# Optimization experiments

Measured on AMD Instinct MI355X. Metric: run time of the kernel, lower is better.

## Reference

```python
import jax, jax.numpy as jnp
import numpy as np

N_EMBD = 1024
N_HEAD = 16
HEAD_SIZE = N_EMBD // N_HEAD


def setup_inputs() -> dict:
    key = jax.random.key(0)
    k_x, k_w, k_b = jax.random.split(key, 3)
    B, T, C = 2, 2048, N_EMBD
    x = jax.random.normal(k_x, (B, T, C), dtype=jnp.float32)
    # Linear(n_embd, 3*n_embd): weight [C, 3C] (applied as x @ W), bias [3C]
    w_qkv = jax.random.normal(k_w, (C, 3 * C), dtype=jnp.float32) * (1.0 / np.sqrt(C))
    b_qkv = jax.random.normal(k_b, (3 * C,), dtype=jnp.float32) * 0.02
    return {"x": x, "w_qkv": w_qkv, "b_qkv": b_qkv}


def reference(x, w_qkv, b_qkv):
    B, T, C = x.shape
    H, D = N_HEAD, HEAD_SIZE
    qkv = x @ w_qkv + b_qkv                      # [B, T, 3C]
    q, k, v = jnp.split(qkv, 3, axis=-1)         # each [B, T, C]
    # [B, T, C] -> [B, H, T, D]
    q = q.reshape(B, T, H, D).transpose(0, 2, 1, 3)
    k = k.reshape(B, T, H, D).transpose(0, 2, 1, 3)
    v = v.reshape(B, T, H, D).transpose(0, 2, 1, 3)
    scores = jnp.einsum('bhqd,bhkd->bhqk', q, k) / jnp.sqrt(jnp.float32(D))
    causal = jnp.tril(jnp.ones((T, T), dtype=bool))  # allow j <= i
    scores = jnp.where(causal[None, None, :, :], scores, -jnp.inf)
    weights = jax.nn.softmax(scores, axis=-1)    # [B, H, T, T]
    out = jnp.einsum('bhqk,bhkd->bhqd', weights, v)
    out = out.transpose(0, 2, 1, 3).reshape(B, T, C)
    return out
```

## Files before the change

kernel.cpp:

```cpp
#include <hip/hip_runtime.h>
#include <hip/hip_bf16.h>


#define CDIM  1024
#define C3    3072
#define HS    64
#define TLEN  2048
#define KVT   64
#define SCL   0.1803368801111204f

typedef __attribute__((ext_vector_type(8))) short bf16x8;
typedef __attribute__((ext_vector_type(4))) float f32x4;
typedef __attribute__((ext_vector_type(4))) unsigned short u16x4;

__device__ __forceinline__ unsigned short f2b(float f) {
    unsigned u = __float_as_uint(f);
    unsigned r = (u + 0x7FFFu + ((u >> 16) & 1u)) >> 16;
    return (unsigned short)r;
}
__device__ __forceinline__ float b2f(unsigned short u) {
    return __uint_as_float(((unsigned)u) << 16);
}
__device__ __forceinline__ float fexp2(float x) {
    return __builtin_amdgcn_exp2f(x);
}
__device__ __forceinline__ unsigned pkbf(float a, float b) {
    float2 f; f.x = a; f.y = b;
    __hip_bfloat162 h = __float22bfloat162_rn(f);
    union { __hip_bfloat162 h2; unsigned u; } c;
    c.h2 = h;
    return c.u;
}
__device__ __forceinline__ void gl_lds16(const unsigned short* g, unsigned short* l) {
    __builtin_amdgcn_global_load_lds((const __attribute__((address_space(1))) void*)g,
                                     (__attribute__((address_space(3))) void*)l, 16, 0, 0);
}
__device__ __forceinline__ int detect_bf(const void* bias, int lane) {
    unsigned w = ((const unsigned*)bias)[lane];
    unsigned e = (w >> 7) & 0xFF;
    unsigned long long m = __ballot(e >= 100 && e <= 135);
    return __popcll(m) >= 48;
}

__device__ __forceinline__ void plswap(unsigned x, unsigned& y0, unsigned& y1) {
    unsigned aa = x, bb = x;
    asm("v_permlane32_swap_b32 %0, %1" : "+v"(aa), "+v"(bb));
    asm("v_permlane16_swap_b32 %0, %1" : "+v"(aa), "+v"(bb));
    y0 = aa; y1 = bb;
}
__device__ __forceinline__ bf16x8 xfrag(unsigned x00, unsigned x01,
                                        unsigned x10, unsigned x11, int qsel) {
    unsigned y000, y100, y001, y101, y010, y110, y011, y111;
    plswap(x00, y000, y100);
    plswap(x01, y001, y101);
    plswap(x10, y010, y110);
    plswap(x11, y011, y111);
    union { unsigned u[4]; bf16x8 v; } r;
    r.u[0] = qsel ? y010 : y000;
    r.u[1] = qsel ? y011 : y001;
    r.u[2] = qsel ? y110 : y100;
    r.u[3] = qsel ? y111 : y101;
    return r.v;
}

__global__ __launch_bounds__(256) void k_prep(const void* __restrict__ w,
                                              const void* __restrict__ x,
                                              const void* __restrict__ bias,
                                              unsigned short* __restrict__ wt,
                                              unsigned short* __restrict__ xb) {
    __shared__ unsigned short tile[64 * 66];
    int t = threadIdx.x;
    int isbf = detect_bf(bias, t & 63);
    int bid = blockIdx.x;

    {
        int n0 = (bid % 48) * 64;
        int k0 = (bid / 48) * 64;
        for (int i = 0; i < 16; ++i) {
            int idx = t + i * 256;
            int r = idx >> 6, c = idx & 63;
            unsigned short v;
            if (isbf) v = ((const unsigned short*)w)[(k0 + r) * C3 + n0 + c];
            else      v = f2b(((const float*)w)[(k0 + r) * C3 + n0 + c]);
            tile[r * 66 + c] = v;
        }
        __syncthreads();
        for (int i = 0; i < 16; ++i) {
            int idx = t + i * 256;
            int r = idx >> 6, c = idx & 63;
            wt[(n0 + r) * CDIM + k0 + c] = tile[c * 66 + r];
        }
    }
    if (!isbf) {
        const float* s = (const float*)x;
        unsigned* d = (unsigned*)xb;
        for (int sb = bid; sb < 2048; sb += 768) {
            int base = sb * 1024;
            for (int j = t; j < 1024; j += 256) {
                int idx = base + j;
                float a = s[2 * idx], b = s[2 * idx + 1];
                d[idx] = (unsigned)f2b(a) | ((unsigned)f2b(b) << 16);
            }
        }
    }
}

__global__ __launch_bounds__(256, 3) void k_gemm_qkv(const void* __restrict__ xraw,
                                                     const unsigned short* __restrict__ xb,
                                                     const void* __restrict__ biasraw,
                                                     const unsigned short* __restrict__ Bt,
                                                     unsigned short* __restrict__ qk,
                                                     unsigned short* __restrict__ k2,
                                                     unsigned short* __restrict__ v2) {
    __shared__ __align__(16) unsigned short As[2 * 128 * 32];
    __shared__ __align__(16) unsigned short Bs[2 * 128 * 32];
    int tid  = threadIdx.x;
    int lane = tid & 63, wv = tid >> 6;
    int quad = lane >> 4, l16 = lane & 15;
    int isbf = detect_bf(biasraw, lane);
    const unsigned short* A = isbf ? (const unsigned short*)xraw : xb;

    int lin = blockIdx.x + 24 * blockIdx.y;
    int swz = (lin & 7) * 96 + (lin >> 3);
    int m0 = (swz / 24) * 128, n0 = (swz % 24) * 128;
    int wm = (wv >> 1) * 64, wn = (wv & 1) * 64;

    f32x4 acc[4][4] = {};

    int r0 = tid >> 2;
    int g0 = (((tid & 3) ^ (r0 & 3)) * 8);
    const unsigned short* a0 = A  + (m0 + r0) * CDIM + g0;
    const unsigned short* b0 = Bt + (n0 + r0) * CDIM + g0;
    unsigned short* dA = As + tid * 8;
    unsigned short* dB = Bs + tid * 8;

    int sw4 = l16 & 3;
    int aro = (wm + l16) * 32 + ((quad ^ sw4) * 8);
    int bro = (wn + l16) * 32 + ((quad ^ sw4) * 8);

    gl_lds16(a0,                 dA);
    gl_lds16(a0 + 64 * CDIM,     dA + 2048);
    gl_lds16(b0,                 dB);
    gl_lds16(b0 + 64 * CDIM,     dB + 2048);
    gl_lds16(a0 + 32,            dA + 4096);
    gl_lds16(a0 + 64 * CDIM + 32, dA + 4096 + 2048);
    gl_lds16(b0 + 32,            dB + 4096);
    gl_lds16(b0 + 64 * CDIM + 32, dB + 4096 + 2048);
    asm volatile("s_waitcnt vmcnt(4)" ::: "memory");
    __builtin_amdgcn_s_barrier();

    #pragma unroll 2
    for (int kt = 0; kt < 32; ++kt) {
        int cur = kt & 1;
        const unsigned short* Ac = As + cur * 4096;
        const unsigned short* Bc = Bs + cur * 4096;

        bf16x8 af[4], bfv[4];
        #pragma unroll
        for (int mt = 0; mt < 4; ++mt)
            af[mt] = *(const bf16x8*)&Ac[aro + mt * 512];
        #pragma unroll
        for (int nt = 0; nt < 4; ++nt)
            bfv[nt] = *(const bf16x8*)&Bc[bro + nt * 512];

        __builtin_amdgcn_s_setprio(1);
        #pragma unroll
        for (int mt = 0; mt < 4; ++mt)
            #pragma unroll
            for (int nt = 0; nt < 4; ++nt)
                acc[mt][nt] = __builtin_amdgcn_mfma_f32_16x16x32_bf16(af[mt], bfv[nt], acc[mt][nt], 0, 0, 0);
        __builtin_amdgcn_s_setprio(0);

        __builtin_amdgcn_s_barrier();
        if (kt < 30) {
            int koff = (kt + 2) * 32;
            unsigned short* tA = As + cur * 4096;
            unsigned short* tB = Bs + cur * 4096;
            gl_lds16(a0 + koff,            tA + tid * 8);
            gl_lds16(a0 + 64 * CDIM + koff, tA + tid * 8 + 2048);
            gl_lds16(b0 + koff,            tB + tid * 8);
            gl_lds16(b0 + 64 * CDIM + koff, tB + tid * 8 + 2048);
            asm volatile("s_waitcnt vmcnt(4)" ::: "memory");
        } else {
            asm volatile("s_waitcnt vmcnt(0)" ::: "memory");
        }
        __builtin_amdgcn_s_barrier();
    }

    if (n0 < 1024) {
        for (int mt = 0; mt < 4; ++mt) {
            int row = m0 + wm + mt * 16 + quad * 4;
            for (int nt = 0; nt < 4; ++nt) {
                int col = n0 + wn + nt * 16 + l16;
                float bv = isbf ? b2f(((const unsigned short*)biasraw)[col])
                                : ((const float*)biasraw)[col];
                for (int i = 0; i < 4; ++i)
                    qk[(row + i) * 2048 + col] = f2b(acc[mt][nt][i] + bv);
            }
        }
    } else if (n0 < 2048) {
        for (int mt = 0; mt < 4; ++mt) {
            int row = m0 + wm + mt * 16 + quad * 4;
            int tq = row & 2047, b = row >> 11;
            for (int nt = 0; nt < 4; ++nt) {
                int col = n0 + wn + nt * 16 + l16;
                float bv = isbf ? b2f(((const unsigned short*)biasraw)[col])
                                : ((const float*)biasraw)[col];
                int c = col - 1024;
                int hh = c >> 6, d = c & 63;
                int base = ((b * 16 + hh) * 32 + (tq >> 6)) * 4096
                         + ((tq >> 5) & 1) * 2048 + ((tq >> 4) & 1) * 1024
                         + (d >> 5) * 512 + ((d >> 3) & 3) * 128
                         + (tq & 15) * 8 + (d & 7);
                for (int i = 0; i < 4; ++i)
                    k2[base + i * 8] = f2b(acc[mt][nt][i] + bv);
            }
        }
    } else {
        for (int mt = 0; mt < 4; ++mt) {
            int row = m0 + wm + mt * 16 + quad * 4;
            int tq = row & 2047, b = row >> 11;
            for (int nt = 0; nt < 4; ++nt) {
                int col = n0 + wn + nt * 16 + l16;
                float bv = isbf ? b2f(((const unsigned short*)biasraw)[col])
                                : ((const float*)biasraw)[col];
                int c = col - 2048;
                int hh = c >> 6, d = c & 63;
                int base = ((b * 16 + hh) * 32 + (tq >> 6)) * 4096
                         + ((tq >> 5) & 1) * 2048 + (d >> 4) * 512
                         + ((tq >> 3) & 3) * 128 + (d & 15) * 8 + (tq & 7);
                u16x4 pk;
                for (int i = 0; i < 4; ++i) pk[i] = f2b(acc[mt][nt][i] + bv);
                *(u16x4*)&v2[base] = pk;
            }
        }
    }
}

__global__ __launch_bounds__(256, 4) void k_attn(const unsigned short* __restrict__ qk,
                                                 const unsigned short* __restrict__ k2,
                                                 const unsigned short* __restrict__ v2,
                                                 const void* __restrict__ biasraw,
                                                 void* __restrict__ outv) {
    __shared__ __align__(16) float SMf[4416];

    int tid  = threadIdx.x;
    int lane = tid & 63, wv = tid >> 6;
    int quad = lane >> 4, l16 = lane & 15;
    int isbf = detect_bf(biasraw, lane);
    int bh = blockIdx.x;
    int g  = 31 - blockIdx.y;
    int b = bh >> 4, h = bh & 15;
    int rowbase = b * TLEN;

    int s_ = wv >> 1;
    int p  = wv & 1;
    int qbase = 64 * g + 32 * s_;
    int T  = g + 1;
    int Tw = T - ((s_ == 0 && p == 1) ? 1 : 0);
    bool dmw = (p == s_);

    bf16x8 qf[2][2];
    for (int qt = 0; qt < 2; ++qt)
        for (int kh = 0; kh < 2; ++kh)
            qf[qt][kh] = *(const bf16x8*)&qk[(rowbase + qbase + qt * 16 + l16) * 2048
                                            + h * HS + kh * 32 + quad * 8];

    f32x4 o[2][4] = {};
    float ls[2] = {0.f, 0.f};

    const unsigned short* kp = k2 + bh * 131072 + p * 2048 + lane * 8;
    const unsigned short* vp = v2 + bh * 131072 + p * 2048 + lane * 8;

    bf16x8 kf00, kf01, kf10, kf11;
    if (Tw > 0) {
        kf00 = *(const bf16x8*)kp;
        kf01 = *(const bf16x8*)(kp + 512);
        kf10 = *(const bf16x8*)(kp + 1024);
        kf11 = *(const bf16x8*)(kp + 1536);
        kp += 4096;
    }

    for (int t = 0; t < Tw; ++t) {
        bf16x8 av0 = *(const bf16x8*)vp;
        bf16x8 av1 = *(const bf16x8*)(vp + 512);
        bf16x8 av2 = *(const bf16x8*)(vp + 1024);
        bf16x8 av3 = *(const bf16x8*)(vp + 1536);
        vp += 4096;

        f32x4 sv[2][2];
        __builtin_amdgcn_s_setprio(1);
        #pragma unroll
        for (int qt = 0; qt < 2; ++qt) {
            f32x4 z0 = {};
            z0 = __builtin_amdgcn_mfma_f32_16x16x32_bf16(kf00, qf[qt][0], z0, 0, 0, 0);
            z0 = __builtin_amdgcn_mfma_f32_16x16x32_bf16(kf01, qf[qt][1], z0, 0, 0, 0);
            sv[qt][0] = z0;
            f32x4 z1 = {};
            z1 = __builtin_amdgcn_mfma_f32_16x16x32_bf16(kf10, qf[qt][0], z1, 0, 0, 0);
            z1 = __builtin_amdgcn_mfma_f32_16x16x32_bf16(kf11, qf[qt][1], z1, 0, 0, 0);
            sv[qt][1] = z1;
        }
        __builtin_amdgcn_s_setprio(0);

        bool pf = (t + 1 < Tw);
        bf16x8 kn00 = *(const bf16x8*)kp;
        bf16x8 kn01 = *(const bf16x8*)(kp + 512);
        bf16x8 kn10 = *(const bf16x8*)(kp + 1024);
        bf16x8 kn11 = *(const bf16x8*)(kp + 1536);
        kp += 4096;

        unsigned sp[2][2][2];
        int kvb = t * KVT + 32 * p;
        if (dmw && (t == T - 1)) {
            #pragma unroll
            for (int qt = 0; qt < 2; ++qt) {
                float psum = 0.f;
                int q = qbase + qt * 16 + l16;
                #pragma unroll
                for (int nt = 0; nt < 2; ++nt) {
                    float pv[4];
                    #pragma unroll
                    for (int i = 0; i < 4; ++i) {
                        float arg = fmaf(sv[qt][nt][i], SCL, -12.0f);
                        int kv = kvb + nt * 16 + quad * 4 + i;
                        if (kv > q) arg = -1e30f;
                        pv[i] = fexp2(arg);
                        psum += pv[i];
                    }
                    sp[qt][nt][0] = pkbf(pv[0], pv[1]);
                    sp[qt][nt][1] = pkbf(pv[2], pv[3]);
                }
                ls[qt] += psum;
            }
        } else {
            #pragma unroll
            for (int qt = 0; qt < 2; ++qt) {
                float psum = 0.f;
                #pragma unroll
                for (int nt = 0; nt < 2; ++nt) {
                    float pv[4];
                    #pragma unroll
                    for (int i = 0; i < 4; ++i) {
                        float arg = fmaf(sv[qt][nt][i], SCL, -12.0f);
                        pv[i] = fexp2(arg);
                        psum += pv[i];
                    }
                    sp[qt][nt][0] = pkbf(pv[0], pv[1]);
                    sp[qt][nt][1] = pkbf(pv[2], pv[3]);
                }
                ls[qt] += psum;
            }
        }

        int qsel = quad & 2;
        bf16x8 f0 = xfrag(sp[0][0][0], sp[0][0][1], sp[0][1][0], sp[0][1][1], qsel);
        bf16x8 f1 = xfrag(sp[1][0][0], sp[1][0][1], sp[1][1][0], sp[1][1][1], qsel);
        __builtin_amdgcn_s_setprio(1);
        o[0][0] = __builtin_amdgcn_mfma_f32_16x16x32_bf16(av0, f0, o[0][0], 0, 0, 0);
        o[1][0] = __builtin_amdgcn_mfma_f32_16x16x32_bf16(av0, f1, o[1][0], 0, 0, 0);
        o[0][1] = __builtin_amdgcn_mfma_f32_16x16x32_bf16(av1, f0, o[0][1], 0, 0, 0);
        o[1][1] = __builtin_amdgcn_mfma_f32_16x16x32_bf16(av1, f1, o[1][1], 0, 0, 0);
        o[0][2] = __builtin_amdgcn_mfma_f32_16x16x32_bf16(av2, f0, o[0][2], 0, 0, 0);
        o[1][2] = __builtin_amdgcn_mfma_f32_16x16x32_bf16(av2, f1, o[1][2], 0, 0, 0);
        o[0][3] = __builtin_amdgcn_mfma_f32_16x16x32_bf16(av3, f0, o[0][3], 0, 0, 0);
        o[1][3] = __builtin_amdgcn_mfma_f32_16x16x32_bf16(av3, f1, o[1][3], 0, 0, 0);
        __builtin_amdgcn_s_setprio(0);

        if (pf) { kf00 = kn00; kf01 = kn01; kf10 = kn10; kf11 = kn11; }
    }

    #pragma unroll
    for (int qt = 0; qt < 2; ++qt) {
        ls[qt] += __shfl_xor(ls[qt], 16);
        ls[qt] += __shfl_xor(ls[qt], 32);
    }
    float* mrg  = SMf;
    float* lbuf = SMf + 4352;

    if (p == 1) {
        #pragma unroll
        for (int qt = 0; qt < 2; ++qt)
            #pragma unroll
            for (int dt = 0; dt < 4; ++dt)
                *(f32x4*)&mrg[s_ * (32 * 68) + (qt * 16 + l16) * 68 + dt * 16 + quad * 4] = o[qt][dt];
        if (quad == 0) {
            lbuf[s_ * 32 + l16]      = ls[0];
            lbuf[s_ * 32 + 16 + l16] = ls[1];
        }
    }
    __syncthreads();
    if (p == 0) {
        #pragma unroll
        for (int qt = 0; qt < 2; ++qt) {
            float lt = ls[qt] + lbuf[s_ * 32 + qt * 16 + l16];
            float inv = 1.0f / lt;
            int q = qbase + qt * 16 + l16;
            if (isbf) {
                unsigned short* out = (unsigned short*)outv;
                #pragma unroll
                for (int dt = 0; dt < 4; ++dt) {
                    f32x4 m = *(const f32x4*)&mrg[s_ * (32 * 68) + (qt * 16 + l16) * 68 + dt * 16 + quad * 4];
                    u16x4 ov;
                    #pragma unroll
                    for (int i = 0; i < 4; ++i) ov[i] = f2b((o[qt][dt][i] + m[i]) * inv);
                    *(u16x4*)&out[(rowbase + q) * CDIM + h * HS + dt * 16 + quad * 4] = ov;
                }
            } else {
                float* out = (float*)outv;
                #pragma unroll
                for (int dt = 0; dt < 4; ++dt) {
                    f32x4 m = *(const f32x4*)&mrg[s_ * (32 * 68) + (qt * 16 + l16) * 68 + dt * 16 + quad * 4];
                    float4 ov;
                    ov.x = (o[qt][dt][0] + m[0]) * inv;
                    ov.y = (o[qt][dt][1] + m[1]) * inv;
                    ov.z = (o[qt][dt][2] + m[2]) * inv;
                    ov.w = (o[qt][dt][3] + m[3]) * inv;
                    *(float4*)&out[(rowbase + q) * CDIM + h * HS + dt * 16 + quad * 4] = ov;
                }
            }
        }
    }
}

extern "C" void kernel_launch(void* const* d_in, const int* in_sizes, int n_in,
                              void* d_out, int out_size, void* d_ws, size_t ws_size,
                              hipStream_t stream) {
    const void* x    = d_in[0];
    const void* w    = d_in[1];
    const void* bias = d_in[2];

    char* ws = (char*)d_ws;
    unsigned short* xb  = (unsigned short*)ws;
    unsigned short* wt  = (unsigned short*)(ws + (8u  << 20));
    unsigned short* qk  = (unsigned short*)(ws + (16u << 20));
    unsigned short* k2  = (unsigned short*)(ws + (32u << 20));
    unsigned short* v2  = (unsigned short*)(ws + (40u << 20));

    k_prep<<<768, 256, 0, stream>>>(w, x, bias, wt, xb);
    k_gemm_qkv<<<dim3(24, 32), 256, 0, stream>>>(x, xb, bias, wt, qk, k2, v2);
    k_attn<<<dim3(32, 32), 256, 0, stream>>>(qk, k2, v2, bias, d_out);
}
```

Measured before the change: 150.9 us.

## Software-pipeline QK^T one tile ahead of softmax in attention loop

The attention inner loop is restructured so the QK^T MFMAs for the next KV tile run while the softmax and PV MFMAs of the current tile are processed. It uses ping-pong score buffers and a 2x manual unroll, which hides MFMA latency behind the exp work. The extra live registers lead to lowering the k_attn launch-bounds occupancy hint from 4 to 3 blocks. The fp32-to-bf16 conversion of x is also vectorized to float4 loads. The prologue now loads K tiles unconditionally, including when Tw is 0, which reads past the valid data and may touch out-of-range memory.

```diff
diff --git a/kernel.cpp b/kernel.cpp
--- a/kernel.cpp
+++ b/kernel.cpp
@@ -92,14 +92,16 @@
         }
     }
     if (!isbf) {
-        const float* s = (const float*)x;
-        unsigned* d = (unsigned*)xb;
+        const float4* s = (const float4*)x;
+        uint2* d = (uint2*)xb;
         for (int sb = bid; sb < 2048; sb += 768) {
-            int base = sb * 1024;
-            for (int j = t; j < 1024; j += 256) {
-                int idx = base + j;
-                float a = s[2 * idx], b = s[2 * idx + 1];
-                d[idx] = (unsigned)f2b(a) | ((unsigned)f2b(b) << 16);
+            int base = sb * 512;
+            for (int j = t; j < 512; j += 256) {
+                float4 v = s[base + j];
+                uint2 o_;
+                o_.x = (unsigned)f2b(v.x) | ((unsigned)f2b(v.y) << 16);
+                o_.y = (unsigned)f2b(v.z) | ((unsigned)f2b(v.w) << 16);
+                d[base + j] = o_;
             }
         }
     }
@@ -237,7 +239,7 @@
     }
 }
 
-__global__ __launch_bounds__(256, 4) void k_attn(const unsigned short* __restrict__ qk,
+__global__ __launch_bounds__(256, 3) void k_attn(const unsigned short* __restrict__ qk,
                                                  const unsigned short* __restrict__ k2,
                                                  const unsigned short* __restrict__ v2,
                                                  const void* __restrict__ biasraw,
@@ -273,46 +275,61 @@
     const unsigned short* vp = v2 + bh * 131072 + p * 2048 + lane * 8;
 
     bf16x8 kf00, kf01, kf10, kf11;
-    if (Tw > 0) {
+    f32x4 svA[2][2], svB[2][2];
+    {
+        bf16x8 k0a = *(const bf16x8*)kp;
+        bf16x8 k0b = *(const bf16x8*)(kp + 512);
+        bf16x8 k0c = *(const bf16x8*)(kp + 1024);
+        bf16x8 k0d = *(const bf16x8*)(kp + 1536);
+        kp += 4096;
         kf00 = *(const bf16x8*)kp;
         kf01 = *(const bf16x8*)(kp + 512);
         kf10 = *(const bf16x8*)(kp + 1024);
         kf11 = *(const bf16x8*)(kp + 1536);
         kp += 4096;
-    }
-
-    for (int t = 0; t < Tw; ++t) {
+        #pragma unroll
+        for (int qt = 0; qt < 2; ++qt) {
+            f32x4 z0 = {};
+            z0 = __builtin_amdgcn_mfma_f32_16x16x32_bf16(k0a, qf[qt][0], z0, 0, 0, 0);
+            z0 = __builtin_amdgcn_mfma_f32_16x16x32_bf16(k0b, qf[qt][1], z0, 0, 0, 0);
+            svA[qt][0] = z0;
+            f32x4 z1 = {};
+            z1 = __builtin_amdgcn_mfma_f32_16x16x32_bf16(k0c, qf[qt][0], z1, 0, 0, 0);
+            z1 = __builtin_amdgcn_mfma_f32_16x16x32_bf16(k0d, qf[qt][1], z1, 0, 0, 0);
+            svA[qt][1] = z1;
+        }
+    }
+
+    auto trip = [&](f32x4 (&svin)[2][2], f32x4 (&svout)[2][2], int tt) {
         bf16x8 av0 = *(const bf16x8*)vp;
         bf16x8 av1 = *(const bf16x8*)(vp + 512);
         bf16x8 av2 = *(const bf16x8*)(vp + 1024);
         bf16x8 av3 = *(const bf16x8*)(vp + 1536);
         vp += 4096;
 
-        f32x4 sv[2][2];
         __builtin_amdgcn_s_setprio(1);
         #pragma unroll
         for (int qt = 0; qt < 2; ++qt) {
             f32x4 z0 = {};
             z0 = __builtin_amdgcn_mfma_f32_16x16x32_bf16(kf00, qf[qt][0], z0, 0, 0, 0);
             z0 = __builtin_amdgcn_mfma_f32_16x16x32_bf16(kf01, qf[qt][1], z0, 0, 0, 0);
-            sv[qt][0] = z0;
+            svout[qt][0] = z0;
             f32x4 z1 = {};
             z1 = __builtin_amdgcn_mfma_f32_16x16x32_bf16(kf10, qf[qt][0], z1, 0, 0, 0);
             z1 = __builtin_amdgcn_mfma_f32_16x16x32_bf16(kf11, qf[qt][1], z1, 0, 0, 0);
-            sv[qt][1] = z1;
+            svout[qt][1] = z1;
         }
         __builtin_amdgcn_s_setprio(0);
 
-        bool pf = (t + 1 < Tw);
-        bf16x8 kn00 = *(const bf16x8*)kp;
-        bf16x8 kn01 = *(const bf16x8*)(kp + 512);
-        bf16x8 kn10 = *(const bf16x8*)(kp + 1024);
-        bf16x8 kn11 = *(const bf16x8*)(kp + 1536);
+        kf00 = *(const bf16x8*)kp;
+        kf01 = *(const bf16x8*)(kp + 512);
+        kf10 = *(const bf16x8*)(kp + 1024);
+        kf11 = *(const bf16x8*)(kp + 1536);
         kp += 4096;
 
         unsigned sp[2][2][2];
-        int kvb = t * KVT + 32 * p;
-        if (dmw && (t == T - 1)) {
+        int kvb = tt * KVT + 32 * p;
+        if (dmw && tt == T - 1) {
             #pragma unroll
             for (int qt = 0; qt < 2; ++qt) {
                 float psum = 0.f;
@@ -322,7 +339,7 @@
                     float pv[4];
                     #pragma unroll
                     for (int i = 0; i < 4; ++i) {
-                        float arg = fmaf(sv[qt][nt][i], SCL, -12.0f);
+                        float arg = fmaf(svin[qt][nt][i], SCL, -12.0f);
                         int kv = kvb + nt * 16 + quad * 4 + i;
                         if (kv > q) arg = -1e30f;
                         pv[i] = fexp2(arg);
@@ -342,7 +359,7 @@
                     float pv[4];
                     #pragma unroll
                     for (int i = 0; i < 4; ++i) {
-                        float arg = fmaf(sv[qt][nt][i], SCL, -12.0f);
+                        float arg = fmaf(svin[qt][nt][i], SCL, -12.0f);
                         pv[i] = fexp2(arg);
                         psum += pv[i];
                     }
@@ -366,9 +383,14 @@
         o[0][3] = __builtin_amdgcn_mfma_f32_16x16x32_bf16(av3, f0, o[0][3], 0, 0, 0);
         o[1][3] = __builtin_amdgcn_mfma_f32_16x16x32_bf16(av3, f1, o[1][3], 0, 0, 0);
         __builtin_amdgcn_s_setprio(0);
-
-        if (pf) { kf00 = kn00; kf01 = kn01; kf10 = kn10; kf11 = kn11; }
-    }
+    };
+
+    int t = 0;
+    for (; t + 2 <= Tw; t += 2) {
+        trip(svA, svB, t);
+        trip(svB, svA, t + 1);
+    }
+    if (t < Tw) trip(svA, svB, t);
 
     #pragma unroll
     for (int qt = 0; qt < 2; ++qt) {
```

Measured after the change: 148.6 us. Within noise of the previous version (-1.5%).
